# Performance work log

Measured on AMD Instinct MI355X. Metric: run time of the kernel, lower is better.

## Reference

```python
import jax, jax.numpy as jnp
import numpy as np

DIM = 1024
NUM_HEADS = 16
HEAD_DIM = DIM // NUM_HEADS
THETA = 10000.0


def apply_rope(x):
    # x: [B, S, H, D]; Llama-style interleaved rotary pairs.
    S, D = x.shape[1], x.shape[3]
    half = D // 2
    inv_freq = THETA ** (-jnp.arange(half, dtype=jnp.float32) * 2.0 / D)  # [D/2]
    angles = jnp.arange(S, dtype=jnp.float32)[:, None] * inv_freq[None, :]  # [S, D/2]
    cos = jnp.cos(angles)[None, :, None, :]  # [1,S,1,D/2]
    sin = jnp.sin(angles)[None, :, None, :]
    x_even = x[..., 0::2]
    x_odd = x[..., 1::2]
    out_even = x_even * cos - x_odd * sin
    out_odd = x_even * sin + x_odd * cos
    out = jnp.stack([out_even, out_odd], axis=-1).reshape(x.shape)
    return out.astype(x.dtype)


def setup_inputs() -> dict:
    key = jax.random.key(0)
    ks = jax.random.split(key, 5)
    B, S = 2, 2048
    x = jax.random.normal(ks[0], (B, S, DIM), dtype=jnp.float32)
    scale = 1.0 / np.sqrt(DIM)
    Wq = jax.random.normal(ks[1], (DIM, DIM), dtype=jnp.float32) * scale
    Wk = jax.random.normal(ks[2], (DIM, DIM), dtype=jnp.float32) * scale
    Wv = jax.random.normal(ks[3], (DIM, DIM), dtype=jnp.float32) * scale
    Wo = jax.random.normal(ks[4], (DIM, DIM), dtype=jnp.float32) * scale
    return {"x": x, "Wq": Wq, "Wk": Wk, "Wv": Wv, "Wo": Wo}


def reference(x, Wq, Wk, Wv, Wo):
    B, S, _ = x.shape
    # torch Linear: y = x @ W^T
    q = (x @ Wq.T).reshape(B, S, NUM_HEADS, HEAD_DIM)
    k = (x @ Wk.T).reshape(B, S, NUM_HEADS, HEAD_DIM)
    v = (x @ Wv.T).reshape(B, S, NUM_HEADS, HEAD_DIM)
    q = apply_rope(q)
    k = apply_rope(k)
    # causal SDPA, scale = 1/sqrt(head_dim)
    scale = 1.0 / np.sqrt(HEAD_DIM).astype(np.float32)
    scores = jnp.einsum("bqhd,bkhd->bhqk", q, k) * scale  # [B,H,S,S]
    causal = jnp.tril(jnp.ones((S, S), dtype=bool))
    scores = jnp.where(causal[None, None], scores, jnp.finfo(scores.dtype).min)
    attn = jax.nn.softmax(scores, axis=-1)
    y = jnp.einsum("bhqk,bkhd->bqhd", attn, v).reshape(B, S, DIM)
    return y @ Wo.T
```

## Files before the change

kernel.cpp:

```cpp
#include <hip/hip_runtime.h>
#include <hip/hip_bf16.h>

typedef __attribute__((ext_vector_type(8))) __bf16 bf16x8;
typedef __attribute__((ext_vector_type(4))) __bf16 bf16x4;
typedef __attribute__((ext_vector_type(4))) float f32x4;
typedef __attribute__((ext_vector_type(16))) float f32x16;
typedef __attribute__((ext_vector_type(2))) unsigned int uint2v;
typedef __attribute__((ext_vector_type(4))) unsigned int uint4v;

#define DIM 1024
#define SLEN 2048
#define NH 16
#define HD 64

__device__ __forceinline__ f32x4 MFMA(bf16x8 a, bf16x8 b, f32x4 c) {
    return __builtin_amdgcn_mfma_f32_16x16x32_bf16(a, b, c, 0, 0, 0);
}
__device__ __forceinline__ f32x16 MFMA32(bf16x8 a, bf16x8 b, f32x16 c) {
    return __builtin_amdgcn_mfma_f32_32x32x16_bf16(a, b, c, 0, 0, 0);
}
__device__ __forceinline__ unsigned pack_bf16(float a, float b) {
    unsigned short ua = __builtin_bit_cast(unsigned short, (__bf16)a);
    unsigned short ub = __builtin_bit_cast(unsigned short, (__bf16)b);
    return ((unsigned)ub << 16) | (unsigned)ua;
}

__global__ __launch_bounds__(256) void cvt_bf16(const float* __restrict__ in,
                                                __bf16* __restrict__ out, int n) {
    int i = (blockIdx.x * blockDim.x + threadIdx.x) * 8;
    if (i >= n) return;
    f32x4 a = *reinterpret_cast<const f32x4*>(in + i);
    f32x4 b = *reinterpret_cast<const f32x4*>(in + i + 4);
    bf16x8 o;
#pragma unroll
    for (int j = 0; j < 4; ++j) { o[j] = (__bf16)a[j]; o[j + 4] = (__bf16)b[j]; }
    *reinterpret_cast<bf16x8*>(out + i) = o;
}

__global__ __launch_bounds__(256) void cvt_w4(const float* __restrict__ w0,
                                              const float* __restrict__ w1,
                                              const float* __restrict__ w2,
                                              const float* __restrict__ w3,
                                              __bf16* __restrict__ o0,
                                              __bf16* __restrict__ o1,
                                              __bf16* __restrict__ o2,
                                              __bf16* __restrict__ o3) {
    int s = blockIdx.y;
    const float* in = s == 0 ? w0 : s == 1 ? w1 : s == 2 ? w2 : w3;
    __bf16* out = s == 0 ? o0 : s == 1 ? o1 : s == 2 ? o2 : o3;
    int i = (blockIdx.x * blockDim.x + threadIdx.x) * 8;
    f32x4 a = *reinterpret_cast<const f32x4*>(in + i);
    f32x4 b = *reinterpret_cast<const f32x4*>(in + i + 4);
    bf16x8 o;
#pragma unroll
    for (int j = 0; j < 4; ++j) { o[j] = (__bf16)a[j]; o[j + 4] = (__bf16)b[j]; }
    *reinterpret_cast<bf16x8*>(out + i) = o;
}

__global__ __launch_bounds__(256) void rope2(__bf16* __restrict__ q,
                                             __bf16* __restrict__ k) {
    __bf16* t = blockIdx.y == 0 ? q : k;
    const float scale = blockIdx.y == 0 ? 0.18033688011112042f : 1.0f;
    int idx = blockIdx.x * blockDim.x + threadIdx.x;
    int row = idx >> 9;
    int p = idx & 511;
    int head = p >> 5;
    int j = p & 31;
    int s = row & (SLEN - 1);
    float inv = expf(-0.28782313662425574f * (float)j);
    float angle = (float)s * inv;
    float sn, cs;
    sincosf(angle, &sn, &cs);
    size_t base = (size_t)row * DIM + head * HD + 2 * j;
    float e = (float)t[base], o = (float)t[base + 1];
    t[base] = (__bf16)((e * cs - o * sn) * scale);
    t[base + 1] = (__bf16)((e * sn + o * cs) * scale);
}

__global__ __launch_bounds__(256) void gemm_qkv(const __bf16* __restrict__ X,
                                                const __bf16* __restrict__ Wq,
                                                const __bf16* __restrict__ Wk,
                                                const __bf16* __restrict__ Wv,
                                                __bf16* __restrict__ Qo,
                                                __bf16* __restrict__ Ko,
                                                __bf16* __restrict__ Vt) {
    __shared__ alignas(16) __bf16 Alds[128 * 64];
    __shared__ alignas(16) __bf16 Blds[128 * 64];
    const int tid = threadIdx.x;
    const int lane = tid & 63;
    const int w = tid >> 6;
    const int wr = w >> 1, wc = w & 1;
    const int l15 = lane & 15, lhi = lane >> 4;
    const int l7 = l15 & 7;
    const int m0 = blockIdx.y * 128;
    const int n0g = blockIdx.x * 128;
    const int seg = n0g >> 10;
    const int n0 = n0g & 1023;
    const __bf16* __restrict__ B = seg == 0 ? Wq : seg == 1 ? Wk : Wv;
    const int K = 1024, N = 1024;

    const int lrow = lane >> 3;
    const int scol = ((lane & 7) ^ lrow) * 8;

    f32x4 acc[4][4] = {};

    for (int kt = 0; kt < K; kt += 64) {
#pragma unroll
        for (int c = 0; c < 4; ++c) {
            int r0 = c * 32 + w * 8;
            const __bf16* sa = &X[(size_t)(m0 + r0 + lrow) * K + kt + scol];
            const __bf16* sb = &B[(size_t)(n0 + r0 + lrow) * K + kt + scol];
            __builtin_amdgcn_global_load_lds((const __attribute__((address_space(1))) void*)sa,
                                             (__attribute__((address_space(3))) void*)&Alds[r0 * 64],
                                             16, 0, 0);
            __builtin_amdgcn_global_load_lds((const __attribute__((address_space(1))) void*)sb,
                                             (__attribute__((address_space(3))) void*)&Blds[r0 * 64],
                                             16, 0, 0);
        }
        __syncthreads();
#pragma unroll
        for (int kk = 0; kk < 2; ++kk) {
            bf16x8 af[4], bfr[4];
#pragma unroll
            for (int i = 0; i < 4; ++i) {
                af[i] = *(const bf16x8*)&Alds[(wr * 64 + i * 16 + l15) * 64 + 8 * ((kk * 4 + lhi) ^ l7)];
                bfr[i] = *(const bf16x8*)&Blds[(wc * 64 + i * 16 + l15) * 64 + 8 * ((kk * 4 + lhi) ^ l7)];
            }
            __builtin_amdgcn_s_setprio(1);
#pragma unroll
            for (int i = 0; i < 4; ++i)
#pragma unroll
                for (int j = 0; j < 4; ++j)
                    acc[i][j] = MFMA(af[i], bfr[j], acc[i][j]);
            __builtin_amdgcn_s_setprio(0);
        }
        __syncthreads();
    }
    if (seg < 2) {
        __bf16* __restrict__ O = seg == 0 ? Qo : Ko;
#pragma unroll
        for (int i = 0; i < 4; ++i)
#pragma unroll
            for (int j = 0; j < 4; ++j)
#pragma unroll
                for (int r = 0; r < 4; ++r) {
                    int row = m0 + wr * 64 + i * 16 + lhi * 4 + r;
                    int col = n0 + wc * 64 + j * 16 + l15;
                    O[(size_t)row * N + col] = (__bf16)acc[i][j][r];
                }
    } else {
#pragma unroll
        for (int i = 0; i < 4; ++i)
#pragma unroll
            for (int j = 0; j < 4; ++j) {
                int row = m0 + wr * 64 + i * 16 + lhi * 4;
                int col = n0 + wc * 64 + j * 16 + l15;
                int bb = row >> 11, s = row & 2047;
                int hh = col >> 6, d = col & 63;
                bf16x4 pk;
#pragma unroll
                for (int r = 0; r < 4; ++r) pk[r] = (__bf16)acc[i][j][r];
                *(bf16x4*)&Vt[((size_t)(bb * 16 + hh) * 64 + d) * SLEN + s] = pk;
            }
    }
}

__global__ __launch_bounds__(256) void gemm_o(const __bf16* __restrict__ A,
                                              const __bf16* __restrict__ B,
                                              float* __restrict__ C) {
    __shared__ alignas(16) __bf16 Alds[64 * 64];
    __shared__ alignas(16) __bf16 Blds[128 * 64];
    const int tid = threadIdx.x;
    const int lane = tid & 63;
    const int w = tid >> 6;
    const int wr = w >> 1, wc = w & 1;
    const int l15 = lane & 15, lhi = lane >> 4;
    const int l7 = l15 & 7;
    const int m0 = blockIdx.y * 64;
    const int n0 = blockIdx.x * 128;
    const int K = 1024, N = 1024;

    const int lrow = lane >> 3;
    const int scol = ((lane & 7) ^ lrow) * 8;

    f32x4 acc[2][4] = {};

    for (int kt = 0; kt < K; kt += 64) {
#pragma unroll
        for (int c = 0; c < 2; ++c) {
            int r0 = c * 32 + w * 8;
            const __bf16* sa = &A[(size_t)(m0 + r0 + lrow) * K + kt + scol];
            __builtin_amdgcn_global_load_lds((const __attribute__((address_space(1))) void*)sa,
                                             (__attribute__((address_space(3))) void*)&Alds[r0 * 64],
                                             16, 0, 0);
        }
#pragma unroll
        for (int c = 0; c < 4; ++c) {
            int r0 = c * 32 + w * 8;
            const __bf16* sb = &B[(size_t)(n0 + r0 + lrow) * K + kt + scol];
            __builtin_amdgcn_global_load_lds((const __attribute__((address_space(1))) void*)sb,
                                             (__attribute__((address_space(3))) void*)&Blds[r0 * 64],
                                             16, 0, 0);
        }
        __syncthreads();
#pragma unroll
        for (int kk = 0; kk < 2; ++kk) {
            bf16x8 af[2], bfr[4];
#pragma unroll
            for (int i = 0; i < 2; ++i)
                af[i] = *(const bf16x8*)&Alds[(wr * 32 + i * 16 + l15) * 64 + 8 * ((kk * 4 + lhi) ^ l7)];
#pragma unroll
            for (int j = 0; j < 4; ++j)
                bfr[j] = *(const bf16x8*)&Blds[(wc * 64 + j * 16 + l15) * 64 + 8 * ((kk * 4 + lhi) ^ l7)];
            __builtin_amdgcn_s_setprio(1);
#pragma unroll
            for (int i = 0; i < 2; ++i)
#pragma unroll
                for (int j = 0; j < 4; ++j)
                    acc[i][j] = MFMA(af[i], bfr[j], acc[i][j]);
            __builtin_amdgcn_s_setprio(0);
        }
        __syncthreads();
    }
#pragma unroll
    for (int i = 0; i < 2; ++i)
#pragma unroll
        for (int j = 0; j < 4; ++j)
#pragma unroll
            for (int r = 0; r < 4; ++r) {
                int row = m0 + wr * 32 + i * 16 + lhi * 4 + r;
                int col = n0 + wc * 64 + j * 16 + l15;
                C[(size_t)row * N + col] = acc[i][j][r];
            }
}

__global__ __launch_bounds__(256, 5) void attn_kernel(const __bf16* __restrict__ Q,
                                                      const __bf16* __restrict__ K,
                                                      const __bf16* __restrict__ Vt,
                                                      __bf16* __restrict__ Y) {
    __shared__ __bf16 Klds[2][64 * 64];
    __shared__ __bf16 Vlds[2][64 * 64];

    const int tid = threadIdx.x;
    const int lane = tid & 63;
    const int w = tid >> 6;
    const int qhalf = w & 1, khalf = w >> 1;
    const int l31 = lane & 31;
    const int hi32 = lane >> 5;
    const int l7 = l31 & 7;

    const int id = blockIdx.x;
    const int x = id & 7, jj = id >> 3;
    const int qt = 31 - (jj >> 2);
    const int bh = 4 * x + (jj & 3);
    const int b = bh >> 4, h = bh & 15;

    const int srow = lane >> 3;
    const int scs = (lane & 7) ^ srow;
    const __bf16* skP = K + (size_t)b * SLEN * DIM + h * HD + (size_t)(8 * w + srow) * DIM + scs * 8;
    const __bf16* svP = Vt + (size_t)bh * 64 * SLEN + (size_t)(8 * w + srow) * SLEN + scs * 8;
    const int dA = (8 * w + srow) * 64;

    auto stage = [&](int buf) {
#pragma unroll
        for (int i = 0; i < 2; ++i) {
            __builtin_amdgcn_global_load_lds(
                (const __attribute__((address_space(1))) void*)(skP + (size_t)i * 32 * DIM),
                (__attribute__((address_space(3))) void*)&Klds[buf][dA + i * 32 * 64], 16, 0, 0);
            __builtin_amdgcn_global_load_lds(
                (const __attribute__((address_space(1))) void*)(svP + (size_t)i * 32 * SLEN),
                (__attribute__((address_space(3))) void*)&Vlds[buf][dA + i * 32 * 64], 16, 0, 0);
        }
        skP += 64 * DIM;
        svP += 64;
    };

    const int qloc = qhalf * 32 + l31;
    const int qg = qt * 64 + qloc;
    const size_t qbase = (size_t)(b * SLEN + qg) * DIM + h * HD;
    bf16x8 qf0 = *(const bf16x8*)&Q[qbase + 0 + 8 * hi32];
    bf16x8 qf1 = *(const bf16x8*)&Q[qbase + 16 + 8 * hi32];
    bf16x8 qf2 = *(const bf16x8*)&Q[qbase + 32 + 8 * hi32];
    bf16x8 qf3 = *(const bf16x8*)&Q[qbase + 48 + 8 * hi32];

    const int krowbase = (khalf * 32 + l31) * 64;
    const int koff0 = krowbase + 8 * ((0 + hi32) ^ l7);
    const int koff1 = krowbase + 8 * ((2 + hi32) ^ l7);
    const int koff2 = krowbase + 8 * ((4 + hi32) ^ l7);
    const int koff3 = krowbase + 8 * ((6 + hi32) ^ l7);
    const int vrow0 = l31 * 64, vrow1 = (32 + l31) * 64;
    const int voff00 = vrow0 + 8 * ((4 * khalf + 0 + hi32) ^ l7);
    const int voff01 = vrow0 + 8 * ((4 * khalf + 2 + hi32) ^ l7);
    const int voff10 = vrow1 + 8 * ((4 * khalf + 0 + hi32) ^ l7);
    const int voff11 = vrow1 + 8 * ((4 * khalf + 2 + hi32) ^ l7);

    bf16x8 ones;
#pragma unroll
    for (int t = 0; t < 8; ++t) ones[t] = (__bf16)1.0f;

    f32x16 acc0 = {}, acc1 = {};
    f32x16 accL = {};

    const int nkt = qt + 1;
    stage(0);
    for (int kt = 0; kt < nkt; ++kt) {
        const int cur = kt & 1;
        __syncthreads();
        if (kt + 1 < nkt) stage(cur ^ 1);
        const __bf16* Kc = Klds[cur];
        const __bf16* Vc = Vlds[cur];

        f32x16 S = {};
        __builtin_amdgcn_s_setprio(1);
        S = MFMA32(*(const bf16x8*)&Kc[koff0], qf0, S);
        S = MFMA32(*(const bf16x8*)&Kc[koff1], qf1, S);
        S = MFMA32(*(const bf16x8*)&Kc[koff2], qf2, S);
        S = MFMA32(*(const bf16x8*)&Kc[koff3], qf3, S);
        __builtin_amdgcn_s_setprio(0);

        if (kt == qt) {
#pragma unroll
            for (int r = 0; r < 16; ++r) {
                const int krow = (r & 3) + 8 * (r >> 2) + 4 * hi32 + 32 * khalf;
                if (krow > qloc) S[r] = -1e30f;
            }
        }
        float p[16];
#pragma unroll
        for (int r = 0; r < 16; ++r) p[r] = exp2f(S[r] - 16.0f);

        bf16x8 pf[2];
#pragma unroll
        for (int ss = 0; ss < 2; ++ss) {
            unsigned P01 = pack_bf16(p[8 * ss + 0], p[8 * ss + 1]);
            unsigned P23 = pack_bf16(p[8 * ss + 2], p[8 * ss + 3]);
            unsigned Q01 = pack_bf16(p[8 * ss + 4], p[8 * ss + 5]);
            unsigned Q23 = pack_bf16(p[8 * ss + 6], p[8 * ss + 7]);
            uint2v sa = __builtin_amdgcn_permlane32_swap(P01, Q01, false, false);
            uint2v sb = __builtin_amdgcn_permlane32_swap(P23, Q23, false, false);
            uint4v pwv = {sa[0], sb[0], sa[1], sb[1]};
            pf[ss] = __builtin_bit_cast(bf16x8, pwv);
        }

        __builtin_amdgcn_s_setprio(1);
        accL = MFMA32(ones, pf[0], accL);
        accL = MFMA32(ones, pf[1], accL);
        acc0 = MFMA32(*(const bf16x8*)&Vc[voff00], pf[0], acc0);
        acc0 = MFMA32(*(const bf16x8*)&Vc[voff01], pf[1], acc0);
        acc1 = MFMA32(*(const bf16x8*)&Vc[voff10], pf[0], acc1);
        acc1 = MFMA32(*(const bf16x8*)&Vc[voff11], pf[1], acc1);
        __builtin_amdgcn_s_setprio(0);
    }

    float lsum = accL[0];
    float* fbuf = (float*)&Klds[0][0];
    float* lbuf = (float*)&Vlds[0][0];
    __syncthreads();
    if (khalf == 1) {
#pragma unroll
        for (int r = 0; r < 16; ++r) {
            fbuf[(qhalf * 2 + 0) * 1024 + r * 64 + lane] = acc0[r];
            fbuf[(qhalf * 2 + 1) * 1024 + r * 64 + lane] = acc1[r];
        }
        lbuf[qhalf * 64 + lane] = lsum;
    }
    __syncthreads();
    if (khalf == 0) {
#pragma unroll
        for (int r = 0; r < 16; ++r) {
            acc0[r] += fbuf[(qhalf * 2 + 0) * 1024 + r * 64 + lane];
            acc1[r] += fbuf[(qhalf * 2 + 1) * 1024 + r * 64 + lane];
        }
        lsum += lbuf[qhalf * 64 + lane];
        const float inv = 1.0f / lsum;
        const size_t obase = (size_t)(b * SLEN + qg) * DIM + h * HD;
#pragma unroll
        for (int g = 0; g < 4; ++g) {
            bf16x4 o0, o1;
#pragma unroll
            for (int e = 0; e < 4; ++e) {
                o0[e] = (__bf16)(acc0[g * 4 + e] * inv);
                o1[e] = (__bf16)(acc1[g * 4 + e] * inv);
            }
            *(bf16x4*)&Y[obase + 8 * g + 4 * hi32] = o0;
            *(bf16x4*)&Y[obase + 32 + 8 * g + 4 * hi32] = o1;
        }
    }
}

extern "C" void kernel_launch(void* const* d_in, const int* in_sizes, int n_in,
                              void* d_out, int out_size, void* d_ws, size_t ws_size,
                              hipStream_t stream) {
    const float* x = (const float*)d_in[0];
    const float* Wq = (const float*)d_in[1];
    const float* Wk = (const float*)d_in[2];
    const float* Wv = (const float*)d_in[3];
    const float* Wo = (const float*)d_in[4];
    float* out = (float*)d_out;

    const size_t XN = (size_t)4096 * 1024;
    const size_t WN = (size_t)1024 * 1024;

    __bf16* xb = (__bf16*)d_ws;
    __bf16* qb = xb + XN;
    __bf16* kb = qb + XN;
    __bf16* vtb = kb + XN;
    __bf16* wqb = vtb + XN;
    __bf16* wkb = wqb + WN;
    __bf16* wvb = wkb + WN;
    __bf16* wob = wvb + WN;
    __bf16* yb = xb;

    cvt_bf16<<<XN / 8 / 256, 256, 0, stream>>>(x, xb, (int)XN);
    dim3 gw(WN / 8 / 256, 4);
    cvt_w4<<<gw, 256, 0, stream>>>(Wq, Wk, Wv, Wo, wqb, wkb, wvb, wob);

    dim3 gq(24, 32);
    gemm_qkv<<<gq, 256, 0, stream>>>(xb, wqb, wkb, wvb, qb, kb, vtb);

    int pairs = 4096 * (DIM / 2);
    dim3 gr(pairs / 256, 2);
    rope2<<<gr, 256, 0, stream>>>(qb, kb);

    attn_kernel<<<1024, 256, 0, stream>>>(qb, kb, vtb, yb);

    dim3 go(8, 64);
    gemm_o<<<go, 256, 0, stream>>>(yb, wob, out);
}
```

Baseline: 125.2 us.

## Fuse RoPE into QKV GEMM epilogue using precomputed cos/sin table

Removes the standalone rope2 kernel, which re-read and re-wrote Q and K in global memory. RoPE plus the Q scaling is now applied in the QKV GEMM epilogue, using a lane shuffle to fetch each rotary partner and a small cos/sin table built by a new kernel. The attention kernel's launch-bounds occupancy hint also drops from 5 to 4 blocks, which loosens the register limit. The trade-offs are an extra tiny launch, per-element table loads in the epilogue, and possibly lower attention occupancy.

```diff
diff --git a/kernel.cpp b/kernel.cpp
--- a/kernel.cpp
+++ b/kernel.cpp
@@ -23,6 +23,15 @@
     unsigned short ua = __builtin_bit_cast(unsigned short, (__bf16)a);
     unsigned short ub = __builtin_bit_cast(unsigned short, (__bf16)b);
     return ((unsigned)ub << 16) | (unsigned)ua;
+}
+
+__global__ __launch_bounds__(256) void rope_tab(float2* __restrict__ tab) {
+    int i = blockIdx.x * 256 + threadIdx.x;
+    int s = i >> 5, j = i & 31;
+    float inv = expf(-0.28782313662425574f * (float)j);
+    float sn, cs;
+    sincosf((float)s * inv, &sn, &cs);
+    tab[i] = make_float2(cs, sn);
 }
 
 __global__ __launch_bounds__(256) void cvt_bf16(const float* __restrict__ in,
@@ -57,33 +66,14 @@
     *reinterpret_cast<bf16x8*>(out + i) = o;
 }
 
-__global__ __launch_bounds__(256) void rope2(__bf16* __restrict__ q,
-                                             __bf16* __restrict__ k) {
-    __bf16* t = blockIdx.y == 0 ? q : k;
-    const float scale = blockIdx.y == 0 ? 0.18033688011112042f : 1.0f;
-    int idx = blockIdx.x * blockDim.x + threadIdx.x;
-    int row = idx >> 9;
-    int p = idx & 511;
-    int head = p >> 5;
-    int j = p & 31;
-    int s = row & (SLEN - 1);
-    float inv = expf(-0.28782313662425574f * (float)j);
-    float angle = (float)s * inv;
-    float sn, cs;
-    sincosf(angle, &sn, &cs);
-    size_t base = (size_t)row * DIM + head * HD + 2 * j;
-    float e = (float)t[base], o = (float)t[base + 1];
-    t[base] = (__bf16)((e * cs - o * sn) * scale);
-    t[base + 1] = (__bf16)((e * sn + o * cs) * scale);
-}
-
 __global__ __launch_bounds__(256) void gemm_qkv(const __bf16* __restrict__ X,
                                                 const __bf16* __restrict__ Wq,
                                                 const __bf16* __restrict__ Wk,
                                                 const __bf16* __restrict__ Wv,
                                                 __bf16* __restrict__ Qo,
                                                 __bf16* __restrict__ Ko,
-                                                __bf16* __restrict__ Vt) {
+                                                __bf16* __restrict__ Vt,
+                                                const float2* __restrict__ tab) {
     __shared__ alignas(16) __bf16 Alds[128 * 64];
     __shared__ alignas(16) __bf16 Blds[128 * 64];
     const int tid = threadIdx.x;
@@ -138,16 +128,26 @@
     }
     if (seg < 2) {
         __bf16* __restrict__ O = seg == 0 ? Qo : Ko;
-#pragma unroll
-        for (int i = 0; i < 4; ++i)
-#pragma unroll
-            for (int j = 0; j < 4; ++j)
+        const float qscale = seg == 0 ? 0.18033688011112042f : 1.0f;
+        const bool codd = l15 & 1;
+#pragma unroll
+        for (int j = 0; j < 4; ++j) {
+            const int col = n0 + wc * 64 + j * 16 + l15;
+            const int jp = (col & 63) >> 1;
+#pragma unroll
+            for (int i = 0; i < 4; ++i)
 #pragma unroll
                 for (int r = 0; r < 4; ++r) {
                     int row = m0 + wr * 64 + i * 16 + lhi * 4 + r;
-                    int col = n0 + wc * 64 + j * 16 + l15;
-                    O[(size_t)row * N + col] = (__bf16)acc[i][j][r];
+                    int s = row & (SLEN - 1);
+                    float2 cs = tab[s * 32 + jp];
+                    float own = acc[i][j][r];
+                    float oth = __shfl_xor(own, 1);
+                    float res = codd ? (oth * cs.y + own * cs.x)
+                                     : (own * cs.x - oth * cs.y);
+                    O[(size_t)row * N + col] = (__bf16)(res * qscale);
                 }
+        }
     } else {
 #pragma unroll
         for (int i = 0; i < 4; ++i)
@@ -234,7 +234,7 @@
             }
 }
 
-__global__ __launch_bounds__(256, 5) void attn_kernel(const __bf16* __restrict__ Q,
+__global__ __launch_bounds__(256, 4) void attn_kernel(const __bf16* __restrict__ Q,
                                                       const __bf16* __restrict__ K,
                                                       const __bf16* __restrict__ Vt,
                                                       __bf16* __restrict__ Y) {
@@ -409,18 +409,16 @@
     __bf16* wkb = wqb + WN;
     __bf16* wvb = wkb + WN;
     __bf16* wob = wvb + WN;
+    float2* tab = (float2*)(wob + WN);
     __bf16* yb = xb;
 
+    rope_tab<<<256, 256, 0, stream>>>(tab);
     cvt_bf16<<<XN / 8 / 256, 256, 0, stream>>>(x, xb, (int)XN);
     dim3 gw(WN / 8 / 256, 4);
     cvt_w4<<<gw, 256, 0, stream>>>(Wq, Wk, Wv, Wo, wqb, wkb, wvb, wob);
 
     dim3 gq(24, 32);
-    gemm_qkv<<<gq, 256, 0, stream>>>(xb, wqb, wkb, wvb, qb, kb, vtb);
-
-    int pairs = 4096 * (DIM / 2);
-    dim3 gr(pairs / 256, 2);
-    rope2<<<gr, 256, 0, stream>>>(qb, kb);
+    gemm_qkv<<<gq, 256, 0, stream>>>(xb, wqb, wkb, wvb, qb, kb, vtb, tab);
 
     attn_kernel<<<1024, 256, 0, stream>>>(qb, kb, vtb, yb);
 
```

After: 124.4 us. About the same (-0.6%).
